# Kernel tuning notes

Hardware: AMD Instinct MI355X
Metric: run time of the kernel (lower is better)

The kernel has to match this reference:

```python
import jax, jax.numpy as jnp
import numpy as np

B, N, C = 4, 8192, 512
H, Dh, G, R = 8, 64, 64, 2  # heads, dim_head, slice_num, mlp_ratio
EPS_LN = 1e-5
EPS_NORM = 1e-5


def _ln(x, g, b):
    m = jnp.mean(x, axis=-1, keepdims=True)
    v = jnp.var(x, axis=-1, keepdims=True)
    return (x - m) * jax.lax.rsqrt(v + EPS_LN) * g + b


def setup_inputs() -> dict:
    key = jax.random.key(0)
    ks = jax.random.split(key, 16)
    r = lambda k, shp: jax.random.normal(k, shp, jnp.float32) * 0.02
    inner = H * Dh
    return {
        "fx": jax.random.normal(ks[0], (B, N, C), jnp.float32),
        "ln1_g": jnp.ones((C,), jnp.float32), "ln1_b": jnp.zeros((C,), jnp.float32),
        "Wx": r(ks[1], (C, inner)), "bx": jnp.zeros((inner,), jnp.float32),
        "Wfx": r(ks[2], (C, inner)), "bfx": jnp.zeros((inner,), jnp.float32),
        "Wslice": r(ks[3], (Dh, G)), "bslice": jnp.zeros((G,), jnp.float32),
        "temperature": jnp.full((1, H, 1, 1), 0.5, jnp.float32),
        "Wq": r(ks[4], (Dh, Dh)), "Wk": r(ks[5], (Dh, Dh)), "Wv": r(ks[6], (Dh, Dh)),
        "Wout": r(ks[7], (inner, C)), "bout": jnp.zeros((C,), jnp.float32),
        "tln_g": jnp.ones((Dh,), jnp.float32), "tln_b": jnp.zeros((Dh,), jnp.float32),
        "Wm1": r(ks[8], (Dh, R * Dh)), "bm1": jnp.zeros((R * Dh,), jnp.float32),
        "Wm2": r(ks[9], (R * Dh, Dh)), "bm2": jnp.zeros((Dh,), jnp.float32),
    }


def reference(fx, ln1_g, ln1_b, Wx, bx, Wfx, bfx, Wslice, bslice, temperature,
              Wq, Wk, Wv, Wout, bout, tln_g, tln_b, Wm1, bm1, Wm2, bm2):
    fx_norm = _ln(fx, ln1_g, ln1_b)                          # [B,N,C]
    # _forward_slice: project to per-head mid features
    x_mid = (fx_norm @ Wx + bx).reshape(B, N, H, Dh).transpose(0, 2, 1, 3)   # [B,H,N,Dh]
    fx_mid = (fx_norm @ Wfx + bfx).reshape(B, N, H, Dh).transpose(0, 2, 1, 3)
    # _project_token: soft slice assignment + weighted pooling into G tokens
    logits = jnp.einsum('bhnd,dg->bhng', x_mid, Wslice) + bslice
    slice_w = jax.nn.softmax(logits / temperature, axis=-1)  # [B,H,N,G]
    slice_norm = jnp.sum(slice_w, axis=2)                    # [B,H,G]
    slice_tok = jnp.einsum('bhnd,bhng->bhgd', fx_mid, slice_w) / (slice_norm[..., None] + EPS_NORM)
    # attention over the small token set (G tokens)
    q = slice_tok @ Wq
    k = slice_tok @ Wk
    v = slice_tok @ Wv
    scale = Dh ** -0.5
    attn = jax.nn.softmax(jnp.einsum('bhgd,bhpd->bhgp', q, k) * scale, axis=-1)
    out_tok = jnp.einsum('bhgp,bhpd->bhgd', attn, v) + slice_tok
    # token MLP with residual
    h = _ln(out_tok, tln_g, tln_b)
    h = jax.nn.gelu(h @ Wm1 + bm1, approximate=False) @ Wm2 + bm2
    tokens = h + out_tok                                     # [B,H,G,Dh]
    # _deslice: weighted scatter back to N points, merge heads, out projection
    out_x = jnp.einsum('bhgd,bhng->bhnd', tokens, slice_w)
    out_x = out_x.transpose(0, 2, 1, 3).reshape(B, N, H * Dh)
    out = out_x @ Wout + bout
    return out + fx_norm
```

## Files before the change

### kernel.cpp

```cpp
#include <hip/hip_runtime.h>
#include <math.h>

#define B_ 4
#define N_ 8192
#define C_ 512
#define H_ 8
#define M_ (B_ * N_)

typedef __attribute__((ext_vector_type(8))) short bf16x8;
typedef __attribute__((ext_vector_type(4))) float f32x4;
typedef __attribute__((ext_vector_type(8))) unsigned short u16x8;
typedef __attribute__((ext_vector_type(4))) unsigned short u16x4;

__device__ __forceinline__ float b2f(unsigned short u) {
  union { unsigned int i; float f; } v;
  v.i = ((unsigned int)u) << 16;
  return v.f;
}
__device__ __forceinline__ unsigned short f2b(float f) {
  union { float f; unsigned int i; } v;
  v.f = f;
  unsigned int r = v.i + 0x7fff + ((v.i >> 16) & 1);
  return (unsigned short)(r >> 16);
}
__device__ __forceinline__ void gl_lds16(const void* g, void* l) {
  __builtin_amdgcn_global_load_lds(
      (const __attribute__((address_space(1))) unsigned int*)g,
      (__attribute__((address_space(3))) unsigned int*)l, 16, 0, 0);
}

__global__ __launch_bounds__(256) void ln_bf16(
    const float* __restrict__ x, const float* __restrict__ gam,
    const float* __restrict__ bet, unsigned short* __restrict__ y) {
  int wave = threadIdx.x >> 6, lane = threadIdx.x & 63;
  int row = (blockIdx.x << 2) + wave;
  const float4* xr = (const float4*)(x + (size_t)row * C_);
  float4 v0 = xr[lane], v1 = xr[lane + 64];
  float s = v0.x + v0.y + v0.z + v0.w + v1.x + v1.y + v1.z + v1.w;
  float q = v0.x * v0.x + v0.y * v0.y + v0.z * v0.z + v0.w * v0.w +
            v1.x * v1.x + v1.y * v1.y + v1.z * v1.z + v1.w * v1.w;
#pragma unroll
  for (int off = 32; off; off >>= 1) {
    s += __shfl_xor(s, off);
    q += __shfl_xor(q, off);
  }
  float mean = s * (1.0f / C_);
  float var = q * (1.0f / C_) - mean * mean;
  float rstd = rsqrtf(var + 1e-5f);
  const float4* gr = (const float4*)gam;
  const float4* br = (const float4*)bet;
  float4 g0 = gr[lane], g1 = gr[lane + 64];
  float4 b0 = br[lane], b1 = br[lane + 64];
  u16x4 oa, ob;
  oa.x = f2b((v0.x - mean) * rstd * g0.x + b0.x);
  oa.y = f2b((v0.y - mean) * rstd * g0.y + b0.y);
  oa.z = f2b((v0.z - mean) * rstd * g0.z + b0.z);
  oa.w = f2b((v0.w - mean) * rstd * g0.w + b0.w);
  ob.x = f2b((v1.x - mean) * rstd * g1.x + b1.x);
  ob.y = f2b((v1.y - mean) * rstd * g1.y + b1.y);
  ob.z = f2b((v1.z - mean) * rstd * g1.z + b1.z);
  ob.w = f2b((v1.w - mean) * rstd * g1.w + b1.w);
  unsigned short* yr = y + (size_t)row * C_;
  *(u16x4*)(yr + (lane << 2)) = oa;
  *(u16x4*)(yr + 256 + (lane << 2)) = ob;
}

__global__ __launch_bounds__(256) void wconv_t(const float* __restrict__ W,
                                               unsigned short* __restrict__ Wt) {
  __shared__ float tile[64][65];
  int t = threadIdx.x;
  int r0 = (int)blockIdx.y << 6, c0 = (int)blockIdx.x << 6;
  int lr = t >> 4, lc = (t & 15) << 2;
#pragma unroll
  for (int p = 0; p < 4; p++) {
    float4 v = *(const float4*)(W + (size_t)(r0 + lr + p * 16) * 512 + c0 + lc);
    tile[lr + p * 16][lc + 0] = v.x;
    tile[lr + p * 16][lc + 1] = v.y;
    tile[lr + p * 16][lc + 2] = v.z;
    tile[lr + p * 16][lc + 3] = v.w;
  }
  __syncthreads();
  int on = t >> 2, ok = (t & 3) << 4;
  unsigned short tmp[16];
#pragma unroll
  for (int j = 0; j < 16; j++) tmp[j] = f2b(tile[ok + j][on]);
  unsigned short* op = Wt + (size_t)(c0 + on) * 512 + r0 + ok;
#pragma unroll
  for (int j4 = 0; j4 < 4; j4++) *(u16x4*)(op + (j4 << 2)) = *(u16x4*)(tmp + (j4 << 2));
}

__global__ __launch_bounds__(256) void wslice_prep(const float* __restrict__ Ws,
                                                   unsigned short* __restrict__ wf) {
  int t = threadIdx.x;
#pragma unroll
  for (int i = 0; i < 2; i++) {
    int idx = t + i * 256;
    int f = idx >> 6, l = idx & 63;
    int gt = f >> 1, ks = f & 1;
    int g = (gt << 4) + (l & 15);
    int d0 = (ks << 5) + ((l >> 4) << 3);
    unsigned short v[8];
#pragma unroll
    for (int jj = 0; jj < 8; jj++) v[jj] = f2b(Ws[(size_t)(d0 + jj) * 64 + g]);
    *(u16x4*)(wf + idx * 8) = *(u16x4*)v;
    *(u16x4*)(wf + idx * 8 + 4) = *(u16x4*)(v + 4);
  }
}

__global__ __launch_bounds__(256) void wfrag_prep(
    const float* __restrict__ Wq, const float* __restrict__ Wk,
    const float* __restrict__ Wv, const float* __restrict__ Wm1,
    const float* __restrict__ Wm2, unsigned short* __restrict__ wfr) {
  int t = threadIdx.x;
  for (int task = t; task < 56 * 64; task += 256) {
    int fid = task >> 6, l = task & 63;
    const float* W;
    int stride, ct, ks;
    if (fid < 24) {
      W = (fid < 8) ? Wq : (fid < 16) ? Wk : Wv;
      int e = fid & 7;
      ct = e >> 1;
      ks = e & 1;
      stride = 64;
    } else if (fid < 40) {
      W = Wm1;
      int e = fid - 24;
      ct = e >> 1;
      ks = e & 1;
      stride = 128;
    } else {
      W = Wm2;
      int e = fid - 40;
      ct = e >> 2;
      ks = e & 3;
      stride = 64;
    }
    int d0 = (ks << 5) + ((l >> 4) << 3);
    int c = (ct << 4) + (l & 15);
    unsigned short v[8];
#pragma unroll
    for (int j = 0; j < 8; j++) v[j] = f2b(W[(size_t)(d0 + j) * stride + c]);
    *(u16x4*)(wfr + task * 8) = *(u16x4*)v;
    *(u16x4*)(wfr + task * 8 + 4) = *(u16x4*)(v + 4);
  }
}

__global__ __launch_bounds__(256) void tokfrag_prep(
    const float* __restrict__ tokens, unsigned short* __restrict__ wtokf) {
  int bh = blockIdx.x, t = threadIdx.x, w = t >> 6, l = t & 63;
  const float* tp = tokens + ((size_t)bh << 12);
#pragma unroll
  for (int fid = w; fid < 8; fid += 4) {
    int mt = fid >> 1, ks = fid & 1;
    int d = (mt << 4) + (l & 15);
    int g0 = (ks << 5) + ((l >> 4) << 3);
    unsigned short v[8];
#pragma unroll
    for (int j = 0; j < 8; j++) v[j] = f2b(tp[(g0 + j) * 64 + d]);
    unsigned short* op = wtokf + (((size_t)bh << 3) + fid) * 512 + (l << 3);
    *(u16x4*)op = *(u16x4*)v;
    *(u16x4*)(op + 4) = *(u16x4*)(v + 4);
  }
}

template <int DEC, bool BIASROW, bool OUTBF, bool RES>
__global__ __launch_bounds__(256) void gemm_bf16(
    const unsigned short* __restrict__ A, const unsigned short* __restrict__ Bt,
    const float* __restrict__ bias, const unsigned short* __restrict__ resid,
    void* __restrict__ Cout, size_t ldC) {
  __shared__ unsigned short lds[8192];
  const int t = threadIdx.x;
  const int w = t >> 6, l = t & 63;
  int bid = blockIdx.x;
  int xcd = bid & 7, q = bid >> 3;
  int bm, bn;
  if (DEC == 0) {
    bm = ((xcd << 5) + (q >> 2)) << 7;
    bn = (q & 3) << 7;
  } else {
    bn = ((xcd << 5) + (q >> 2)) << 7;
    bm = (q & 3) << 7;
  }
  const int wm = (w >> 1) << 6, wn = (w & 1) << 6;
  f32x4 acc[4][4];
#pragma unroll
  for (int mt = 0; mt < 4; mt++)
#pragma unroll
    for (int nt = 0; nt < 4; nt++) acc[mt][nt] = (f32x4){0.f, 0.f, 0.f, 0.f};

  const int srow = t >> 2;
  const int scol = (t & 3) << 3;
  const unsigned short* gA0 = A + (size_t)(bm + srow) * 512 + scol;
  const unsigned short* gA1 = A + (size_t)(bm + 64 + srow) * 512 + scol;
  const unsigned short* gB0 = Bt + (size_t)(bn + srow) * 512 + scol;
  const unsigned short* gB1 = Bt + (size_t)(bn + 64 + srow) * 512 + scol;
  const int fr = l & 15, fq = (l >> 4) << 3;

  for (int k0 = 0; k0 < 512; k0 += 32) {
    gl_lds16(gA0 + k0, lds + (w << 9));
    gl_lds16(gA1 + k0, lds + 2048 + (w << 9));
    gl_lds16(gB0 + k0, lds + 4096 + (w << 9));
    gl_lds16(gB1 + k0, lds + 6144 + (w << 9));
    __syncthreads();
    bf16x8 af[4], bfr[4];
#pragma unroll
    for (int mt = 0; mt < 4; mt++)
      af[mt] = *(const bf16x8*)&lds[(wm + mt * 16 + fr) * 32 + fq];
#pragma unroll
    for (int nt = 0; nt < 4; nt++)
      bfr[nt] = *(const bf16x8*)&lds[4096 + (wn + nt * 16 + fr) * 32 + fq];
#pragma unroll
    for (int mt = 0; mt < 4; mt++)
#pragma unroll
      for (int nt = 0; nt < 4; nt++)
        acc[mt][nt] = __builtin_amdgcn_mfma_f32_16x16x32_bf16(
            af[mt], bfr[nt], acc[mt][nt], 0, 0, 0);
    __syncthreads();
  }

  const int col0 = bn + wn + (l & 15);
  const int row0 = bm + wm + ((l >> 4) << 2);
#pragma unroll
  for (int mt = 0; mt < 4; mt++) {
#pragma unroll
    for (int j = 0; j < 4; j++) {
      int row = row0 + mt * 16 + j;
#pragma unroll
      for (int nt = 0; nt < 4; nt++) {
        int col = col0 + nt * 16;
        float v = acc[mt][nt][j] + (BIASROW ? bias[row] : bias[col]);
        if (RES) v += b2f(resid[(size_t)row * ldC + col]);
        if (OUTBF)
          ((unsigned short*)Cout)[(size_t)row * ldC + col] = f2b(v);
        else
          ((float*)Cout)[(size_t)row * ldC + col] = v;
      }
    }
  }
}

__global__ __launch_bounds__(256) void slice_mfma(
    unsigned short* __restrict__ xw, const unsigned short* __restrict__ wf,
    const float* __restrict__ bslice, const float* __restrict__ temp) {
  __shared__ unsigned short xs[4096];
  int t = threadIdx.x, w = t >> 6, l = t & 63;
  int blk = blockIdx.x;
  size_t base = (size_t)blk << 12;
  {
    int srow = t >> 2;
    const unsigned short* gp = xw + base + srow * 64 + ((t & 3) << 4);
    u16x8 a = *(const u16x8*)gp;
    u16x8 b = *(const u16x8*)(gp + 8);
    int sl0 = (t & 3) << 1, swz = srow & 7;
    *(u16x8*)&xs[srow * 64 + ((sl0 ^ swz) << 3)] = a;
    *(u16x8*)&xs[srow * 64 + (((sl0 + 1) ^ swz) << 3)] = b;
  }
  bf16x8 wsf[4][2];
#pragma unroll
  for (int gt = 0; gt < 4; gt++)
#pragma unroll
    for (int ks = 0; ks < 2; ks++)
      wsf[gt][ks] = *(const bf16x8*)(wf + (((gt << 1) + ks) * 64 + l) * 8);
  __syncthreads();

  int xr = (w << 4) + (l & 15);
  f32x4 acc[4];
#pragma unroll
  for (int gt = 0; gt < 4; gt++) acc[gt] = (f32x4){0.f, 0.f, 0.f, 0.f};
#pragma unroll
  for (int ks = 0; ks < 2; ks++) {
    int slot = (ks << 2) + (l >> 4);
    bf16x8 xf = *(const bf16x8*)&xs[xr * 64 + ((slot ^ (xr & 7)) << 3)];
#pragma unroll
    for (int gt = 0; gt < 4; gt++)
      acc[gt] = __builtin_amdgcn_mfma_f32_16x16x32_bf16(wsf[gt][ks], xf,
                                                        acc[gt], 0, 0, 0);
  }

  int gxr = (blk << 6) + xr;
  float invt = 1.0f / temp[gxr & 7];
  int qq = l >> 4;
  float lg[16];
  float mx = -1e30f;
#pragma unroll
  for (int gt = 0; gt < 4; gt++)
#pragma unroll
    for (int r = 0; r < 4; r++) {
      float v = (acc[gt][r] + bslice[(gt << 4) + (qq << 2) + r]) * invt;
      lg[(gt << 2) + r] = v;
      mx = fmaxf(mx, v);
    }
  mx = fmaxf(mx, __shfl_xor(mx, 16));
  mx = fmaxf(mx, __shfl_xor(mx, 32));
  float ssum = 0.f;
#pragma unroll
  for (int i = 0; i < 16; i++) {
    lg[i] = expf(lg[i] - mx);
    ssum += lg[i];
  }
  ssum += __shfl_xor(ssum, 16);
  ssum += __shfl_xor(ssum, 32);
  float inv = 1.0f / ssum;
  __syncthreads();
#pragma unroll
  for (int gt = 0; gt < 4; gt++) {
    int slot = (gt << 1) + (qq >> 1);
    int off = ((slot ^ (xr & 7)) << 3) + ((qq & 1) << 2);
    u16x4 pk;
    pk.x = f2b(lg[(gt << 2) + 0] * inv);
    pk.y = f2b(lg[(gt << 2) + 1] * inv);
    pk.z = f2b(lg[(gt << 2) + 2] * inv);
    pk.w = f2b(lg[(gt << 2) + 3] * inv);
    *(u16x4*)&xs[xr * 64 + off] = pk;
  }
  __syncthreads();
  {
    int rr = (w << 4) + (l >> 2);
    int sl = (l & 3) << 1, swz = rr & 7;
    u16x8 o0 = *(const u16x8*)&xs[rr * 64 + ((sl ^ swz) << 3)];
    u16x8 o1 = *(const u16x8*)&xs[rr * 64 + (((sl + 1) ^ swz) << 3)];
    unsigned short* op = xw + base + rr * 64 + ((l & 3) << 4);
    *(u16x8*)op = o0;
    *(u16x8*)(op + 8) = o1;
  }
}

__global__ __launch_bounds__(256) void pool_mfma(
    const unsigned short* __restrict__ sw, const unsigned short* __restrict__ fxT,
    float* __restrict__ tok_part, float* __restrict__ norm_part) {
  __shared__ unsigned short wT[4096];
  int bid = blockIdx.x;
  int bh = bid >> 4, c = bid & 15;
  int b = bh >> 3, h = bh & 7;
  int t = threadIdx.x, w = t >> 6, l = t & 63;
  int n0 = c << 9;
  const int fr15 = l & 15, fs = l >> 4;
  f32x4 acc[4];
#pragma unroll
  for (int gt = 0; gt < 4; gt++) acc[gt] = (f32x4){0.f, 0.f, 0.f, 0.f};
  float nacc[4] = {0.f, 0.f, 0.f, 0.f};

  const unsigned short* fxrow =
      fxT + (size_t)(h * 64 + w * 16 + fr15) * 32768 + b * N_ + n0 + (fs << 3);

  for (int nn = 0; nn < 512; nn += 64) {
    size_t srow = ((size_t)(b * N_ + n0 + nn + l) * 8 + h) << 6;
    u16x8 a0 = *(const u16x8*)(sw + srow + w * 16);
    u16x8 a1 = *(const u16x8*)(sw + srow + w * 16 + 8);
    __syncthreads();
#pragma unroll
    for (int j = 0; j < 16; j++) {
      int g = (w << 4) + j;
      unsigned short v = (j < 8) ? (unsigned short)a0[j] : (unsigned short)a1[j - 8];
      wT[(g << 6) + (((l >> 3) ^ (g & 7)) << 3) + (l & 7)] = v;
    }
    __syncthreads();
#pragma unroll
    for (int kk = 0; kk < 2; kk++) {
      bf16x8 bfrag = *(const bf16x8*)(fxrow + nn + (kk << 5));
#pragma unroll
      for (int gt = 0; gt < 4; gt++) {
        int g = (gt << 4) + fr15;
        int slot = (kk << 2) + fs;
        bf16x8 af = *(const bf16x8*)&wT[(g << 6) + ((slot ^ (g & 7)) << 3)];
        acc[gt] = __builtin_amdgcn_mfma_f32_16x16x32_bf16(af, bfrag, acc[gt], 0, 0, 0);
        if (w == 0) {
#pragma unroll
          for (int j = 0; j < 8; j++) nacc[gt] += b2f((unsigned short)af[j]);
        }
      }
    }
  }
  float* op = tok_part + ((size_t)bid << 12);
#pragma unroll
  for (int gt = 0; gt < 4; gt++)
#pragma unroll
    for (int rr = 0; rr < 4; rr++)
      op[((gt << 4) + (fs << 2) + rr) * 64 + (w << 4) + fr15] = acc[gt][rr];
  if (w == 0) {
#pragma unroll
    for (int gt = 0; gt < 4; gt++) {
      float s = nacc[gt];
      s += __shfl_xor(s, 16);
      s += __shfl_xor(s, 32);
      if (l < 16) norm_part[(bid << 6) + (gt << 4) + l] = s;
    }
  }
}

__global__ __launch_bounds__(256) void tok_reduce(
    const float* __restrict__ tok_part, const float* __restrict__ norm_part,
    float* __restrict__ stG) {
  int blk = blockIdx.x;
  int bh = blk >> 2, qq = blk & 3;
  int t = threadIdx.x;
  int e = (qq << 10) + (t << 2);
  int g = e >> 6;
  float s = 0.f;
  const float* np = norm_part + ((size_t)bh << 10);
#pragma unroll
  for (int c = 0; c < 16; c++) s += np[(c << 6) + g];
  float4 acc = make_float4(0.f, 0.f, 0.f, 0.f);
  const float* tp = tok_part + ((size_t)bh << 16) + e;
#pragma unroll
  for (int c = 0; c < 16; c++) {
    float4 v = *(const float4*)(tp + (c << 12));
    acc.x += v.x;
    acc.y += v.y;
    acc.z += v.z;
    acc.w += v.w;
  }
  float inv = 1.0f / (s + 1e-5f);
  acc.x *= inv;
  acc.y *= inv;
  acc.z *= inv;
  acc.w *= inv;
  *(float4*)(stG + ((size_t)bh << 12) + e) = acc;
}

__device__ __forceinline__ float gelu_exact(float x) {
  return 0.5f * x * (1.0f + erff(x * 0.70710678118654752f));
}

__global__ __launch_bounds__(256) void token_mfma(
    const float* __restrict__ stG, const unsigned short* __restrict__ wfr,
    const float* __restrict__ tg, const float* __restrict__ tb,
    const float* __restrict__ bm1, const float* __restrict__ bm2,
    float* __restrict__ tokens) {
  __shared__ __align__(16) char smem[54272];
  unsigned short* stb = (unsigned short*)smem;
  float* st32 = (float*)(smem + 9216);
  unsigned short* hmld = (unsigned short*)(smem + 9216);
  unsigned short* qld = (unsigned short*)(smem + 26624);
  unsigned short* kld = (unsigned short*)(smem + 35840);
  unsigned short* vtl = (unsigned short*)(smem + 45056);

  int bh = blockIdx.x, t = threadIdx.x, w = t >> 6, l = t & 63;
  const int fr = l & 15, fq = l >> 4;

  {
    int r = t >> 2, c0 = (t & 3) << 4;
    const float* gp = stG + ((size_t)bh << 12) + r * 64 + c0;
    float4 a = *(const float4*)gp;
    float4 b = *(const float4*)(gp + 4);
    float4 c = *(const float4*)(gp + 8);
    float4 d = *(const float4*)(gp + 12);
    *(float4*)&st32[r * 68 + c0] = a;
    *(float4*)&st32[r * 68 + c0 + 4] = b;
    *(float4*)&st32[r * 68 + c0 + 8] = c;
    *(float4*)&st32[r * 68 + c0 + 12] = d;
    unsigned short tv[16];
    tv[0] = f2b(a.x); tv[1] = f2b(a.y); tv[2] = f2b(a.z); tv[3] = f2b(a.w);
    tv[4] = f2b(b.x); tv[5] = f2b(b.y); tv[6] = f2b(b.z); tv[7] = f2b(b.w);
    tv[8] = f2b(c.x); tv[9] = f2b(c.y); tv[10] = f2b(c.z); tv[11] = f2b(c.w);
    tv[12] = f2b(d.x); tv[13] = f2b(d.y); tv[14] = f2b(d.z); tv[15] = f2b(d.w);
    *(u16x8*)&stb[r * 72 + c0] = *(u16x8*)tv;
    *(u16x8*)&stb[r * 72 + c0 + 8] = *(u16x8*)(tv + 8);
  }
  __syncthreads();

  const int orow = (w << 4) + (fq << 2);

  {
    bf16x8 af[2];
#pragma unroll
    for (int ks = 0; ks < 2; ks++)
      af[ks] = *(const bf16x8*)&stb[((w << 4) + fr) * 72 + (ks << 5) + (fq << 3)];
    f32x4 aq[4], ak[4], av[4];
#pragma unroll
    for (int ct = 0; ct < 4; ct++) {
      aq[ct] = (f32x4){0.f, 0.f, 0.f, 0.f};
      ak[ct] = (f32x4){0.f, 0.f, 0.f, 0.f};
      av[ct] = (f32x4){0.f, 0.f, 0.f, 0.f};
    }
#pragma unroll
    for (int ct = 0; ct < 4; ct++)
#pragma unroll
      for (int ks = 0; ks < 2; ks++) {
        bf16x8 bq = *(const bf16x8*)&wfr[(((ct << 1) + ks) * 64 + l) * 8];
        aq[ct] = __builtin_amdgcn_mfma_f32_16x16x32_bf16(af[ks], bq, aq[ct], 0, 0, 0);
      }
#pragma unroll
    for (int ct = 0; ct < 4; ct++)
#pragma unroll
      for (int ks = 0; ks < 2; ks++) {
        bf16x8 bk = *(const bf16x8*)&wfr[((8 + (ct << 1) + ks) * 64 + l) * 8];
        ak[ct] = __builtin_amdgcn_mfma_f32_16x16x32_bf16(af[ks], bk, ak[ct], 0, 0, 0);
      }
#pragma unroll
    for (int ct = 0; ct < 4; ct++)
#pragma unroll
      for (int ks = 0; ks < 2; ks++) {
        bf16x8 bv = *(const bf16x8*)&wfr[((16 + (ct << 1) + ks) * 64 + l) * 8];
        av[ct] = __builtin_amdgcn_mfma_f32_16x16x32_bf16(af[ks], bv, av[ct], 0, 0, 0);
      }
#pragma unroll
    for (int ct = 0; ct < 4; ct++) {
#pragma unroll
      for (int rr = 0; rr < 4; rr++) {
        qld[(orow + rr) * 72 + (ct << 4) + fr] = f2b(aq[ct][rr]);
        kld[(orow + rr) * 72 + (ct << 4) + fr] = f2b(ak[ct][rr]);
      }
      u16x4 vp;
      vp.x = f2b(av[ct][0]);
      vp.y = f2b(av[ct][1]);
      vp.z = f2b(av[ct][2]);
      vp.w = f2b(av[ct][3]);
      *(u16x4*)&vtl[((ct << 4) + fr) * 72 + orow] = vp;
    }
  }
  __syncthreads();

  {
    bf16x8 aq[2];
#pragma unroll
    for (int ks = 0; ks < 2; ks++)
      aq[ks] = *(const bf16x8*)&qld[((w << 4) + fr) * 72 + (ks << 5) + (fq << 3)];
    f32x4 accs[4];
#pragma unroll
    for (int nt = 0; nt < 4; nt++) accs[nt] = (f32x4){0.f, 0.f, 0.f, 0.f};
#pragma unroll
    for (int nt = 0; nt < 4; nt++)
#pragma unroll
      for (int ks = 0; ks < 2; ks++) {
        bf16x8 bk = *(const bf16x8*)&kld[((nt << 4) + fr) * 72 + (ks << 5) + (fq << 3)];
        accs[nt] = __builtin_amdgcn_mfma_f32_16x16x32_bf16(aq[ks], bk, accs[nt], 0, 0, 0);
      }
#pragma unroll
    for (int rr = 0; rr < 4; rr++) {
      float v0 = accs[0][rr] * 0.125f, v1 = accs[1][rr] * 0.125f;
      float v2 = accs[2][rr] * 0.125f, v3 = accs[3][rr] * 0.125f;
      float mx = fmaxf(fmaxf(v0, v1), fmaxf(v2, v3));
      mx = fmaxf(mx, __shfl_xor(mx, 1));
      mx = fmaxf(mx, __shfl_xor(mx, 2));
      mx = fmaxf(mx, __shfl_xor(mx, 4));
      mx = fmaxf(mx, __shfl_xor(mx, 8));
      float e0 = expf(v0 - mx), e1 = expf(v1 - mx);
      float e2 = expf(v2 - mx), e3 = expf(v3 - mx);
      float ss = e0 + e1 + e2 + e3;
      ss += __shfl_xor(ss, 1);
      ss += __shfl_xor(ss, 2);
      ss += __shfl_xor(ss, 4);
      ss += __shfl_xor(ss, 8);
      float inv = 1.0f / ss;
      stb[(orow + rr) * 72 + 0 * 16 + fr] = f2b(e0 * inv);
      stb[(orow + rr) * 72 + 1 * 16 + fr] = f2b(e1 * inv);
      stb[(orow + rr) * 72 + 2 * 16 + fr] = f2b(e2 * inv);
      stb[(orow + rr) * 72 + 3 * 16 + fr] = f2b(e3 * inv);
    }
  }
  __syncthreads();

  float o16[4][4];
  {
    bf16x8 ap[2];
#pragma unroll
    for (int ks = 0; ks < 2; ks++)
      ap[ks] = *(const bf16x8*)&stb[((w << 4) + fr) * 72 + (ks << 5) + (fq << 3)];
    f32x4 acco[4];
#pragma unroll
    for (int ct = 0; ct < 4; ct++) acco[ct] = (f32x4){0.f, 0.f, 0.f, 0.f};
#pragma unroll
    for (int ct = 0; ct < 4; ct++)
#pragma unroll
      for (int ks = 0; ks < 2; ks++) {
        bf16x8 bv = *(const bf16x8*)&vtl[((ct << 4) + fr) * 72 + (ks << 5) + (fq << 3)];
        acco[ct] = __builtin_amdgcn_mfma_f32_16x16x32_bf16(ap[ks], bv, acco[ct], 0, 0, 0);
      }
    float tgv[4], tbv[4];
#pragma unroll
    for (int ct = 0; ct < 4; ct++) {
      tgv[ct] = tg[(ct << 4) + fr];
      tbv[ct] = tb[(ct << 4) + fr];
    }
#pragma unroll
    for (int ct = 0; ct < 4; ct++)
#pragma unroll
      for (int rr = 0; rr < 4; rr++)
        o16[ct][rr] = acco[ct][rr] + st32[(orow + rr) * 68 + (ct << 4) + fr];
#pragma unroll
    for (int rr = 0; rr < 4; rr++) {
      float sm = o16[0][rr] + o16[1][rr] + o16[2][rr] + o16[3][rr];
      float sq = o16[0][rr] * o16[0][rr] + o16[1][rr] * o16[1][rr] +
                 o16[2][rr] * o16[2][rr] + o16[3][rr] * o16[3][rr];
      sm += __shfl_xor(sm, 1);
      sm += __shfl_xor(sm, 2);
      sm += __shfl_xor(sm, 4);
      sm += __shfl_xor(sm, 8);
      sq += __shfl_xor(sq, 1);
      sq += __shfl_xor(sq, 2);
      sq += __shfl_xor(sq, 4);
      sq += __shfl_xor(sq, 8);
      float mean = sm * (1.0f / 64.0f);
      float var = sq * (1.0f / 64.0f) - mean * mean;
      float rstd = rsqrtf(var + 1e-5f);
#pragma unroll
      for (int ct = 0; ct < 4; ct++) {
        float hv = (o16[ct][rr] - mean) * rstd * tgv[ct] + tbv[ct];
        qld[(orow + rr) * 72 + (ct << 4) + fr] = f2b(hv);
      }
    }
  }
  __syncthreads();

  {
    bf16x8 ah[2];
#pragma unroll
    for (int ks = 0; ks < 2; ks++)
      ah[ks] = *(const bf16x8*)&qld[((w << 4) + fr) * 72 + (ks << 5) + (fq << 3)];
    f32x4 accm[8];
#pragma unroll
    for (int et = 0; et < 8; et++) accm[et] = (f32x4){0.f, 0.f, 0.f, 0.f};
#pragma unroll
    for (int et = 0; et < 8; et++)
#pragma unroll
      for (int ks = 0; ks < 2; ks++) {
        bf16x8 bm = *(const bf16x8*)&wfr[((24 + (et << 1) + ks) * 64 + l) * 8];
        accm[et] = __builtin_amdgcn_mfma_f32_16x16x32_bf16(ah[ks], bm, accm[et], 0, 0, 0);
      }
#pragma unroll
    for (int et = 0; et < 8; et++) {
      float bv = bm1[(et << 4) + fr];
#pragma unroll
      for (int rr = 0; rr < 4; rr++) {
        float x = accm[et][rr] + bv;
        hmld[(orow + rr) * 136 + (et << 4) + fr] = f2b(gelu_exact(x));
      }
    }
  }
  __syncthreads();

  {
    bf16x8 ahm[4];
#pragma unroll
    for (int ks = 0; ks < 4; ks++)
      ahm[ks] = *(const bf16x8*)&hmld[((w << 4) + fr) * 136 + (ks << 5) + (fq << 3)];
    f32x4 acc2[4];
#pragma unroll
    for (int ct = 0; ct < 4; ct++) acc2[ct] = (f32x4){0.f, 0.f, 0.f, 0.f};
#pragma unroll
    for (int ct = 0; ct < 4; ct++)
#pragma unroll
      for (int ks = 0; ks < 4; ks++) {
        bf16x8 bw = *(const bf16x8*)&wfr[((40 + (ct << 2) + ks) * 64 + l) * 8];
        acc2[ct] = __builtin_amdgcn_mfma_f32_16x16x32_bf16(ahm[ks], bw, acc2[ct], 0, 0, 0);
      }
    float* tout = tokens + ((size_t)bh << 12);
#pragma unroll
    for (int ct = 0; ct < 4; ct++) {
      float bv = bm2[(ct << 4) + fr];
#pragma unroll
      for (int rr = 0; rr < 4; rr++)
        tout[(orow + rr) * 64 + (ct << 4) + fr] = acc2[ct][rr] + bv + o16[ct][rr];
    }
  }
}

__global__ __launch_bounds__(256) void deslice_mfma(
    const unsigned short* __restrict__ wtokf, const unsigned short* __restrict__ sw,
    unsigned short* __restrict__ outx) {
  int bid = blockIdx.x;
  int bh = bid >> 4, c = bid & 15;
  int b = bh >> 3, h = bh & 7;
  int t = threadIdx.x, w = t >> 6, l = t & 63;
  const int fr = l & 15, fq = l >> 4;

  bf16x8 ta[4][2];
  const unsigned short* fp = wtokf + ((size_t)bh << 12);
#pragma unroll
  for (int mt = 0; mt < 4; mt++)
#pragma unroll
    for (int ks = 0; ks < 2; ks++)
      ta[mt][ks] = *(const bf16x8*)(fp + (((mt << 1) + ks) << 9) + (l << 3));

  int n0 = (c << 9) + (w << 7);
#pragma unroll 2
  for (int ntile = 0; ntile < 8; ntile++) {
    int nb = n0 + (ntile << 4);
    size_t rowb = ((size_t)(b * N_ + nb + fr) * 8 + h) << 6;
    bf16x8 b0 = *(const bf16x8*)(sw + rowb + (fq << 3));
    bf16x8 b1 = *(const bf16x8*)(sw + rowb + 32 + (fq << 3));
    f32x4 acc[4];
#pragma unroll
    for (int mt = 0; mt < 4; mt++) acc[mt] = (f32x4){0.f, 0.f, 0.f, 0.f};
#pragma unroll
    for (int mt = 0; mt < 4; mt++) {
      acc[mt] = __builtin_amdgcn_mfma_f32_16x16x32_bf16(ta[mt][0], b0, acc[mt], 0, 0, 0);
      acc[mt] = __builtin_amdgcn_mfma_f32_16x16x32_bf16(ta[mt][1], b1, acc[mt], 0, 0, 0);
    }
    unsigned short* op = outx + rowb + (fq << 2);
#pragma unroll
    for (int mt = 0; mt < 4; mt++) {
      u16x4 pk;
      pk.x = f2b(acc[mt][0]);
      pk.y = f2b(acc[mt][1]);
      pk.z = f2b(acc[mt][2]);
      pk.w = f2b(acc[mt][3]);
      *(u16x4*)(op + (mt << 4)) = pk;
    }
  }
}

extern "C" void kernel_launch(void* const* d_in, const int* in_sizes, int n_in,
                              void* d_out, int out_size, void* d_ws,
                              size_t ws_size, hipStream_t stream) {
  const float* fx = (const float*)d_in[0];
  const float* ln1g = (const float*)d_in[1];
  const float* ln1b = (const float*)d_in[2];
  const float* Wx = (const float*)d_in[3];
  const float* bx = (const float*)d_in[4];
  const float* Wfx = (const float*)d_in[5];
  const float* bfx = (const float*)d_in[6];
  const float* Wsl = (const float*)d_in[7];
  const float* bsl = (const float*)d_in[8];
  const float* temp = (const float*)d_in[9];
  const float* Wq = (const float*)d_in[10];
  const float* Wk = (const float*)d_in[11];
  const float* Wv = (const float*)d_in[12];
  const float* Wout = (const float*)d_in[13];
  const float* bout = (const float*)d_in[14];
  const float* tlng = (const float*)d_in[15];
  const float* tlnb = (const float*)d_in[16];
  const float* Wm1 = (const float*)d_in[17];
  const float* bm1 = (const float*)d_in[18];
  const float* Wm2 = (const float*)d_in[19];
  const float* bm2 = (const float*)d_in[20];
  float* out = (float*)d_out;

  char* p = (char*)d_ws;
  const size_t MC2 = (size_t)M_ * 512 * 2;
  unsigned short* fxn = (unsigned short*)p;  p += MC2;
  unsigned short* buf1 = (unsigned short*)p; p += MC2;
  unsigned short* bufT = (unsigned short*)p; p += MC2;
  unsigned short* WtX = (unsigned short*)p;  p += 512 * 512 * 2;
  unsigned short* WtF = (unsigned short*)p;  p += 512 * 512 * 2;
  unsigned short* WtO = (unsigned short*)p;  p += 512 * 512 * 2;
  unsigned short* wsf = (unsigned short*)p;  p += 8192;
  unsigned short* wfr = (unsigned short*)p;  p += 56 * 512 * 2;
  unsigned short* wtokf = (unsigned short*)p; p += (size_t)32 * 8 * 512 * 2;
  float* tok_part = (float*)p;  p += (size_t)512 * 4096 * 4;
  float* norm_part = (float*)p; p += (size_t)512 * 64 * 4;
  float* tokens = (float*)p;    p += (size_t)32 * 4096 * 4;
  float* stG = (float*)p;       p += (size_t)32 * 4096 * 4;

  ln_bf16<<<M_ / 4, 256, 0, stream>>>(fx, ln1g, ln1b, fxn);
  dim3 wg(8, 8);
  wconv_t<<<wg, 256, 0, stream>>>(Wx, WtX);
  wconv_t<<<wg, 256, 0, stream>>>(Wfx, WtF);
  wconv_t<<<wg, 256, 0, stream>>>(Wout, WtO);
  wslice_prep<<<1, 256, 0, stream>>>(Wsl, wsf);
  wfrag_prep<<<1, 256, 0, stream>>>(Wq, Wk, Wv, Wm1, Wm2, wfr);
  gemm_bf16<0, false, true, false><<<1024, 256, 0, stream>>>(fxn, WtX, bx, nullptr, buf1, 512);
  gemm_bf16<1, true, true, false><<<1024, 256, 0, stream>>>(WtF, fxn, bfx, nullptr, bufT, 32768);
  slice_mfma<<<4096, 256, 0, stream>>>(buf1, wsf, bsl, temp);
  pool_mfma<<<512, 256, 0, stream>>>(buf1, bufT, tok_part, norm_part);
  tok_reduce<<<128, 256, 0, stream>>>(tok_part, norm_part, stG);
  token_mfma<<<32, 256, 0, stream>>>(stG, wfr, tlng, tlnb, bm1, bm2, tokens);
  tokfrag_prep<<<32, 256, 0, stream>>>(tokens, wtokf);
  deslice_mfma<<<512, 256, 0, stream>>>(wtokf, buf1, bufT);
  gemm_bf16<0, false, false, true><<<1024, 256, 0, stream>>>(bufT, WtO, bout, fxn, out, 512);
}
```

Measured before the change: 192.9 us.

## Merge weight prep kernels into one launch and swizzle GEMM LDS layout

Five small weight-conversion kernels (three transposes, slice fragment, token-MLP fragments) are merged into one 193-block launch to cut launch overhead. Separately, the bf16 GEMM now XOR-swizzles the 16-byte column slot when staging A/B tiles into LDS and applies the matching swizzle on fragment reads, to reduce LDS bank conflicts. The swizzle has to stay consistent between the write and read sides. The merged prep kernel allocates shared memory in every block, including the one that does not need it.

```diff
diff --git a/kernel.cpp b/kernel.cpp
--- a/kernel.cpp
+++ b/kernel.cpp
@@ -65,83 +65,84 @@
   *(u16x4*)(yr + 256 + (lane << 2)) = ob;
 }
 
-__global__ __launch_bounds__(256) void wconv_t(const float* __restrict__ W,
-                                               unsigned short* __restrict__ Wt) {
-  __shared__ float tile[64][65];
-  int t = threadIdx.x;
-  int r0 = (int)blockIdx.y << 6, c0 = (int)blockIdx.x << 6;
-  int lr = t >> 4, lc = (t & 15) << 2;
-#pragma unroll
-  for (int p = 0; p < 4; p++) {
-    float4 v = *(const float4*)(W + (size_t)(r0 + lr + p * 16) * 512 + c0 + lc);
-    tile[lr + p * 16][lc + 0] = v.x;
-    tile[lr + p * 16][lc + 1] = v.y;
-    tile[lr + p * 16][lc + 2] = v.z;
-    tile[lr + p * 16][lc + 3] = v.w;
-  }
-  __syncthreads();
-  int on = t >> 2, ok = (t & 3) << 4;
-  unsigned short tmp[16];
-#pragma unroll
-  for (int j = 0; j < 16; j++) tmp[j] = f2b(tile[ok + j][on]);
-  unsigned short* op = Wt + (size_t)(c0 + on) * 512 + r0 + ok;
-#pragma unroll
-  for (int j4 = 0; j4 < 4; j4++) *(u16x4*)(op + (j4 << 2)) = *(u16x4*)(tmp + (j4 << 2));
-}
-
-__global__ __launch_bounds__(256) void wslice_prep(const float* __restrict__ Ws,
-                                                   unsigned short* __restrict__ wf) {
-  int t = threadIdx.x;
-#pragma unroll
-  for (int i = 0; i < 2; i++) {
-    int idx = t + i * 256;
-    int f = idx >> 6, l = idx & 63;
-    int gt = f >> 1, ks = f & 1;
-    int g = (gt << 4) + (l & 15);
-    int d0 = (ks << 5) + ((l >> 4) << 3);
-    unsigned short v[8];
-#pragma unroll
-    for (int jj = 0; jj < 8; jj++) v[jj] = f2b(Ws[(size_t)(d0 + jj) * 64 + g]);
-    *(u16x4*)(wf + idx * 8) = *(u16x4*)v;
-    *(u16x4*)(wf + idx * 8 + 4) = *(u16x4*)(v + 4);
-  }
-}
-
-__global__ __launch_bounds__(256) void wfrag_prep(
+__global__ __launch_bounds__(256) void prep_all(
+    const float* __restrict__ Wx, const float* __restrict__ Wfx,
+    const float* __restrict__ Wout, const float* __restrict__ Wsl,
     const float* __restrict__ Wq, const float* __restrict__ Wk,
     const float* __restrict__ Wv, const float* __restrict__ Wm1,
-    const float* __restrict__ Wm2, unsigned short* __restrict__ wfr) {
-  int t = threadIdx.x;
-  for (int task = t; task < 56 * 64; task += 256) {
-    int fid = task >> 6, l = task & 63;
-    const float* W;
-    int stride, ct, ks;
-    if (fid < 24) {
-      W = (fid < 8) ? Wq : (fid < 16) ? Wk : Wv;
-      int e = fid & 7;
-      ct = e >> 1;
-      ks = e & 1;
-      stride = 64;
-    } else if (fid < 40) {
-      W = Wm1;
-      int e = fid - 24;
-      ct = e >> 1;
-      ks = e & 1;
-      stride = 128;
-    } else {
-      W = Wm2;
-      int e = fid - 40;
-      ct = e >> 2;
-      ks = e & 3;
-      stride = 64;
-    }
-    int d0 = (ks << 5) + ((l >> 4) << 3);
-    int c = (ct << 4) + (l & 15);
-    unsigned short v[8];
-#pragma unroll
-    for (int j = 0; j < 8; j++) v[j] = f2b(W[(size_t)(d0 + j) * stride + c]);
-    *(u16x4*)(wfr + task * 8) = *(u16x4*)v;
-    *(u16x4*)(wfr + task * 8 + 4) = *(u16x4*)(v + 4);
+    const float* __restrict__ Wm2, unsigned short* __restrict__ WtX,
+    unsigned short* __restrict__ WtF, unsigned short* __restrict__ WtO,
+    unsigned short* __restrict__ wsf, unsigned short* __restrict__ wfr) {
+  __shared__ float tile[64][65];
+  int blk = blockIdx.x, t = threadIdx.x;
+  if (blk < 192) {
+    int which = blk >> 6, sub = blk & 63;
+    const float* W = (which == 0) ? Wx : (which == 1) ? Wfx : Wout;
+    unsigned short* Wt = (which == 0) ? WtX : (which == 1) ? WtF : WtO;
+    int r0 = (sub >> 3) << 6, c0 = (sub & 7) << 6;
+    int lr = t >> 4, lc = (t & 15) << 2;
+#pragma unroll
+    for (int p = 0; p < 4; p++) {
+      float4 v = *(const float4*)(W + (size_t)(r0 + lr + p * 16) * 512 + c0 + lc);
+      tile[lr + p * 16][lc + 0] = v.x;
+      tile[lr + p * 16][lc + 1] = v.y;
+      tile[lr + p * 16][lc + 2] = v.z;
+      tile[lr + p * 16][lc + 3] = v.w;
+    }
+    __syncthreads();
+    int on = t >> 2, ok = (t & 3) << 4;
+    unsigned short tmp[16];
+#pragma unroll
+    for (int j = 0; j < 16; j++) tmp[j] = f2b(tile[ok + j][on]);
+    unsigned short* op = Wt + (size_t)(c0 + on) * 512 + r0 + ok;
+#pragma unroll
+    for (int j4 = 0; j4 < 4; j4++)
+      *(u16x4*)(op + (j4 << 2)) = *(u16x4*)(tmp + (j4 << 2));
+  } else {
+#pragma unroll
+    for (int i = 0; i < 2; i++) {
+      int idx = t + i * 256;
+      int f = idx >> 6, l = idx & 63;
+      int gt = f >> 1, ks = f & 1;
+      int g = (gt << 4) + (l & 15);
+      int d0 = (ks << 5) + ((l >> 4) << 3);
+      unsigned short v[8];
+#pragma unroll
+      for (int jj = 0; jj < 8; jj++) v[jj] = f2b(Wsl[(size_t)(d0 + jj) * 64 + g]);
+      *(u16x4*)(wsf + idx * 8) = *(u16x4*)v;
+      *(u16x4*)(wsf + idx * 8 + 4) = *(u16x4*)(v + 4);
+    }
+    for (int task = t; task < 56 * 64; task += 256) {
+      int fid = task >> 6, l = task & 63;
+      const float* W;
+      int stride, ct, ks;
+      if (fid < 24) {
+        W = (fid < 8) ? Wq : (fid < 16) ? Wk : Wv;
+        int e = fid & 7;
+        ct = e >> 1;
+        ks = e & 1;
+        stride = 64;
+      } else if (fid < 40) {
+        W = Wm1;
+        int e = fid - 24;
+        ct = e >> 1;
+        ks = e & 1;
+        stride = 128;
+      } else {
+        W = Wm2;
+        int e = fid - 40;
+        ct = e >> 2;
+        ks = e & 3;
+        stride = 64;
+      }
+      int d0 = (ks << 5) + ((l >> 4) << 3);
+      int c = (ct << 4) + (l & 15);
+      unsigned short v[8];
+#pragma unroll
+      for (int j = 0; j < 8; j++) v[j] = f2b(W[(size_t)(d0 + j) * stride + c]);
+      *(u16x4*)(wfr + task * 8) = *(u16x4*)v;
+      *(u16x4*)(wfr + task * 8 + 4) = *(u16x4*)(v + 4);
+    }
   }
 }
 
@@ -189,12 +190,13 @@
     for (int nt = 0; nt < 4; nt++) acc[mt][nt] = (f32x4){0.f, 0.f, 0.f, 0.f};
 
   const int srow = t >> 2;
-  const int scol = (t & 3) << 3;
+  const int scol = (((t & 3) ^ ((t >> 3) & 3)) << 3);
   const unsigned short* gA0 = A + (size_t)(bm + srow) * 512 + scol;
   const unsigned short* gA1 = A + (size_t)(bm + 64 + srow) * 512 + scol;
   const unsigned short* gB0 = Bt + (size_t)(bn + srow) * 512 + scol;
   const unsigned short* gB1 = Bt + (size_t)(bn + 64 + srow) * 512 + scol;
-  const int fr = l & 15, fq = (l >> 4) << 3;
+  const int fr = l & 15;
+  const int pslot = (((l >> 4) ^ ((l >> 1) & 3)) << 3);
 
   for (int k0 = 0; k0 < 512; k0 += 32) {
     gl_lds16(gA0 + k0, lds + (w << 9));
@@ -205,10 +207,10 @@
     bf16x8 af[4], bfr[4];
 #pragma unroll
     for (int mt = 0; mt < 4; mt++)
-      af[mt] = *(const bf16x8*)&lds[(wm + mt * 16 + fr) * 32 + fq];
+      af[mt] = *(const bf16x8*)&lds[(wm + mt * 16 + fr) * 32 + pslot];
 #pragma unroll
     for (int nt = 0; nt < 4; nt++)
-      bfr[nt] = *(const bf16x8*)&lds[4096 + (wn + nt * 16 + fr) * 32 + fq];
+      bfr[nt] = *(const bf16x8*)&lds[4096 + (wn + nt * 16 + fr) * 32 + pslot];
 #pragma unroll
     for (int mt = 0; mt < 4; mt++)
 #pragma unroll
@@ -744,12 +746,8 @@
   float* stG = (float*)p;       p += (size_t)32 * 4096 * 4;
 
   ln_bf16<<<M_ / 4, 256, 0, stream>>>(fx, ln1g, ln1b, fxn);
-  dim3 wg(8, 8);
-  wconv_t<<<wg, 256, 0, stream>>>(Wx, WtX);
-  wconv_t<<<wg, 256, 0, stream>>>(Wfx, WtF);
-  wconv_t<<<wg, 256, 0, stream>>>(Wout, WtO);
-  wslice_prep<<<1, 256, 0, stream>>>(Wsl, wsf);
-  wfrag_prep<<<1, 256, 0, stream>>>(Wq, Wk, Wv, Wm1, Wm2, wfr);
+  prep_all<<<193, 256, 0, stream>>>(Wx, Wfx, Wout, Wsl, Wq, Wk, Wv, Wm1, Wm2,
+                                    WtX, WtF, WtO, wsf, wfr);
   gemm_bf16<0, false, true, false><<<1024, 256, 0, stream>>>(fxn, WtX, bx, nullptr, buf1, 512);
   gemm_bf16<1, true, true, false><<<1024, 256, 0, stream>>>(WtF, fxn, bfx, nullptr, bufT, 32768);
   slice_mfma<<<4096, 256, 0, stream>>>(buf1, wsf, bsl, temp);
```

Result: faster. 185.3 us (-4.0%).
